# Kernel tuning notes

Hardware: AMD Instinct MI355X
Metric: run time of the kernel (lower is better)

Reference implementation:

```python
import jax, jax.numpy as jnp
import numpy as np
from jax import lax

B, E, T = 16, 512, 512
H, R = 1024, 32
P = 8192
W = 3            # window_size
MAX_SPAN = 8


def setup_inputs() -> dict:
    key = jax.random.key(0)
    ks = jax.random.split(key, 16)
    s = lambda fan: 1.0 / np.sqrt(fan)
    return {
        'rel_word_x': jax.random.normal(ks[0], (B, E, T), jnp.float32),
        'trig_attn': jax.random.normal(ks[1], (B, T), jnp.float32),
        'batch_idx': jax.random.randint(ks[2], (P,), 0, B),
        'head_index': jax.random.randint(ks[3], (P,), 0, T - MAX_SPAN),
        'head_span': jax.random.randint(ks[4], (P,), 1, MAX_SPAN + 1),
        'tail_index': jax.random.randint(ks[5], (P,), 0, T - MAX_SPAN),
        'tail_span': jax.random.randint(ks[6], (P,), 1, MAX_SPAN + 1),
        'rel_labels': jax.random.randint(ks[7], (P,), 0, R),
        'conv1_w': jax.random.uniform(ks[8], (E, E, W), jnp.float32, -s(E * W), s(E * W)),
        'conv1_b': jnp.zeros((E,), jnp.float32),
        'conv2_w': jax.random.uniform(ks[9], (E, E, W), jnp.float32, -s(E * W), s(E * W)),
        'conv2_b': jnp.zeros((E,), jnp.float32),
        'w1': jax.random.uniform(ks[10], (H, E), jnp.float32, -s(E), s(E)),
        'b1': jnp.zeros((H,), jnp.float32),
        'w2': jax.random.uniform(ks[11], (H, H), jnp.float32, -s(H), s(H)),
        'b2': jnp.zeros((H,), jnp.float32),
        'wr': jax.random.uniform(ks[12], (R, H), jnp.float32, -s(H), s(H)),
        'br': jnp.zeros((R,), jnp.float32),
    }


def _conv1d(x, w, b):
    # x: [B,E,T], w: [O,I,W] -> same-length conv (odd W)
    y = lax.conv_general_dilated(x, w, window_strides=(1,), padding=[(W // 2, W // 2)],
                                 dimension_numbers=('NCH', 'OIH', 'NCH'))
    return y + b[None, :, None]


def _span_max(x_bte, bidx, start, span):
    # x_bte: [B,T,E]; ragged span max via fixed-width gather + mask
    offs = jnp.arange(MAX_SPAN)
    pos = start[:, None] + offs[None, :]                  # [P,S]
    vals = x_bte[bidx[:, None], pos]                      # [P,S,E]
    mask = (offs[None, :] < span[:, None])[..., None]     # [P,S,1]
    return jnp.max(jnp.where(mask, vals, -jnp.inf), axis=1)  # [P,E]


def reference(rel_word_x, trig_attn, batch_idx, head_index, head_span,
              tail_index, tail_span, rel_labels,
              conv1_w, conv1_b, conv2_w, conv2_b, w1, b1, w2, b2, wr, br):
    # dropout treated as identity (eval-mode reference)
    x = rel_word_x
    x = jax.nn.relu(_conv1d(x, conv1_w, conv1_b)) + x
    x = jax.nn.relu(_conv1d(x, conv2_w, conv2_b)) + x
    x_bte = jnp.transpose(x, (0, 2, 1))                   # [B,T,E]
    headrep = _span_max(x_bte, batch_idx, head_index, head_span)
    tailrep = _span_max(x_bte, batch_idx, tail_index, tail_span)
    maxed = headrep + tailrep                             # [P,E]
    h = jax.nn.relu(maxed @ w1.T + b1)                    # [P,H]
    h = jax.nn.relu(h @ w2.T + b2)                        # [P,H]
    rel_logits = h @ wr.T + br                            # [P,R]
    return rel_logits, trig_attn, rel_labels
```

## Files before the change

### kernel.cpp

```cpp
#include <hip/hip_runtime.h>

typedef unsigned short u16;
typedef unsigned int u32;
typedef __attribute__((ext_vector_type(4))) float f32x4;
typedef __attribute__((ext_vector_type(8))) __bf16 bf16x8;
typedef __attribute__((ext_vector_type(4))) u16 u16x4;
typedef const __attribute__((address_space(1))) void* as1cv;
typedef __attribute__((address_space(3))) void* as3v;

static __device__ __forceinline__ float bf2f(u16 v) {
  union { u32 u; float f; } x; x.u = ((u32)v) << 16; return x.f;
}
static __device__ __forceinline__ u16 f2bf(float f) {
  union { float f; u32 u; } x; x.f = f;
  u32 r = x.u + 0x7FFFu + ((x.u >> 16) & 1u);
  return (u16)(r >> 16);
}


__global__ void __launch_bounds__(256) k_transpose(const float* __restrict__ x,
                                                   u16* __restrict__ xtp) {
  __shared__ float tile[32][33];
  const int b = blockIdx.z;
  const int t0 = blockIdx.x * 32, e0 = blockIdx.y * 32;
  const int tx = threadIdx.x & 31, ty = threadIdx.x >> 5;
  const float* src = x + (size_t)b * 512 * 512;
#pragma unroll
  for (int i = 0; i < 32; i += 8)
    tile[ty + i][tx] = src[(size_t)(e0 + ty + i) * 512 + t0 + tx];
  __syncthreads();
  u16* dst = xtp + (size_t)b * 514 * 512;
#pragma unroll
  for (int i = 0; i < 32; i += 8)
    dst[(size_t)(t0 + ty + i + 1) * 512 + e0 + tx] = f2bf(tile[tx][ty + i]);
}

__global__ void __launch_bounds__(256) k_prep(
    const float* __restrict__ wa, const float* __restrict__ wb,
    u16* __restrict__ ga, u16* __restrict__ gb,
    const float* __restrict__ w1, const float* __restrict__ w2,
    const float* __restrict__ wr, u16* __restrict__ wdst,
    u16* __restrict__ xtp0, u16* __restrict__ xtp1,
    const float* __restrict__ trig, const int* __restrict__ labels,
    float* __restrict__ out) {
  const int idx = blockIdx.x * 256 + threadIdx.x;
  {
    const float* w = (idx < 262144) ? wa : wb;
    u16* g = (idx < 262144) ? ga : gb;
    const int id = idx & 262143;
    const int o = id >> 9, i = id & 511;
    const float* p = w + (size_t)id * 3;
    g[(size_t)o * 1536 + i]        = f2bf(p[0]);
    g[(size_t)o * 1536 + 512 + i]  = f2bf(p[1]);
    g[(size_t)o * 1536 + 1024 + i] = f2bf(p[2]);
  }
  if (idx < 401408) {
    const int e0 = idx * 4;
    const float* src; int off;
    if (e0 < 524288)       { src = w1; off = e0; }
    else if (e0 < 1572864) { src = w2; off = e0 - 524288; }
    else                   { src = wr; off = e0 - 1572864; }
    const float4 v = *(const float4*)(src + off);
    u16x4 r; r.x = f2bf(v.x); r.y = f2bf(v.y); r.z = f2bf(v.z); r.w = f2bf(v.w);
    *(u16x4*)(wdst + e0) = r;
  }
  if (idx < 262144) out[idx] = 0.f;
  if (idx < 16384) {
    const int b = idx >> 10, rem = idx & 1023;
    const int row = (rem >> 9) ? 513 : 0, e = rem & 511;
    const size_t off = (size_t)b * 514 * 512 + (size_t)row * 512 + e;
    xtp0[off] = 0;
    xtp1[off] = 0;
  }
  if (idx < 8192) {
    out[262144 + idx] = trig[idx];
    out[270336 + idx] = (float)labels[idx];
  }
}

__global__ void __launch_bounds__(256) k_spanmax(const u16* __restrict__ xt2,
    const int* __restrict__ bidx, const int* __restrict__ hidx, const int* __restrict__ hspan,
    const int* __restrict__ tidx, const int* __restrict__ tspan, u16* __restrict__ maxed) {
  const int p = blockIdx.x;
  const int b = bidx[p], h0 = hidx[p], hn = hspan[p], t0 = tidx[p], tn = tspan[p];
  const u32* base = (const u32*)(xt2 + (size_t)b * 512 * 512);
  const int e = threadIdx.x;
  float m0 = -1e30f, m1 = -1e30f, q0 = -1e30f, q1 = -1e30f;
  for (int s = 0; s < hn; ++s) {
    const u32 v = base[(size_t)(h0 + s) * 256 + e];
    m0 = fmaxf(m0, bf2f((u16)v));
    m1 = fmaxf(m1, bf2f((u16)(v >> 16)));
  }
  for (int s = 0; s < tn; ++s) {
    const u32 v = base[(size_t)(t0 + s) * 256 + e];
    q0 = fmaxf(q0, bf2f((u16)v));
    q1 = fmaxf(q1, bf2f((u16)(v >> 16)));
  }
  const u32 r = (u32)f2bf(m0 + q0) | ((u32)f2bf(m1 + q1) << 16);
  ((u32*)(maxed + (size_t)p * 512))[e] = r;
}

template<int BM, int BN, int WM, int WN, int CONV, int RELU, int RESID, int OUTF32,
         int ATOMIC, int SWZ>
__global__ void __launch_bounds__(256, 2) k_gemm(
    const u16* __restrict__ A, int strideA, long long batchA,
    const u16* __restrict__ Bw, int strideB, long long batchB, int K,
    const float* __restrict__ bias,
    const u16* __restrict__ resid, long long batchR,
    void* __restrict__ outp, long long batchO, int strideO,
    int swz_nx, int swz_nyb, int swz_pp) {
  constexpr int FM = BM / (16 * WM);
  constexpr int FN = BN / (16 * WN);
  constexpr int CA = BM / 16, CB = BN / 16;
  __shared__ __align__(16) u16 lds[2][(BM + BN) * 32];
  const int tid = threadIdx.x;
  const int wave = tid >> 6, lane = tid & 63;
  int m0, n0, z;
  if constexpr (SWZ) {
    const int lin = blockIdx.x;
    const int xcd = lin & 7, slot = lin >> 3;
    const int xb = slot % swz_nx;
    const int p  = xcd * swz_pp + slot / swz_nx;
    m0 = (p % swz_nyb) * BM;
    n0 = xb * BN;
    z  = p / swz_nyb;
  } else {
    m0 = blockIdx.y * BM; n0 = blockIdx.x * BN; z = blockIdx.z;
  }
  const u16* Ab = A + (size_t)z * batchA;
  const u16* Bb = Bw + (size_t)z * batchB;
  const int NT = K >> 5;

  auto stage = [&](int t, int buf) {
    const int k0 = t << 5;
    const int arow = CONV ? (k0 >> 9) : 0;
    const int acol = CONV ? (k0 & 511) : k0;
    for (int c = wave; c < CA + CB; c += 4) {
      const u16* gsrc;
      u16* ldst;
      if (c < CA) {
        const int r0 = c << 4;
        ldst = &lds[buf][r0 * 32];
        const int row = m0 + r0 + (lane >> 2) + arow;
        gsrc = Ab + (size_t)row * strideA + acol + ((lane & 3) << 3);
      } else {
        const int r0 = (c - CA) << 4;
        ldst = &lds[buf][BM * 32 + r0 * 32];
        const int row = n0 + r0 + (lane >> 2);
        gsrc = Bb + (size_t)row * strideB + k0 + ((lane & 3) << 3);
      }
      __builtin_amdgcn_global_load_lds((as1cv)gsrc, (as3v)ldst, 16, 0, 0);
    }
  };

  f32x4 acc[FM][FN];
  const f32x4 zero4 = {0.f, 0.f, 0.f, 0.f};
#pragma unroll
  for (int m = 0; m < FM; ++m)
#pragma unroll
    for (int n = 0; n < FN; ++n) acc[m][n] = zero4;

  const int wrow = wave / WN, wcol = wave % WN;
  const int rsel = lane & 15;
  const int kc = (lane >> 4) << 3;

  stage(0, 0);
  __syncthreads();
  int cur = 0;
  for (int t = 0; t < NT; ++t) {
    if (t + 1 < NT) stage(t + 1, cur ^ 1);
    const u16* As = lds[cur];
    const u16* Bs = lds[cur] + BM * 32;
    bf16x8 af[FM], bq[FN];
#pragma unroll
    for (int m = 0; m < FM; ++m)
      af[m] = *(const bf16x8*)&As[(wrow * FM * 16 + m * 16 + rsel) * 32 + kc];
#pragma unroll
    for (int n = 0; n < FN; ++n)
      bq[n] = *(const bf16x8*)&Bs[(wcol * FN * 16 + n * 16 + rsel) * 32 + kc];
#pragma unroll
    for (int m = 0; m < FM; ++m)
#pragma unroll
      for (int n = 0; n < FN; ++n)
        acc[m][n] = __builtin_amdgcn_mfma_f32_16x16x32_bf16(af[m], bq[n], acc[m][n], 0, 0, 0);
    __syncthreads();
    cur ^= 1;
  }

  const int rowbase = m0 + wrow * FM * 16 + ((lane >> 4) << 2);
  const int colbase = n0 + wcol * FN * 16 + rsel;
  float bv[FN];
#pragma unroll
  for (int n = 0; n < FN; ++n)
    bv[n] = (!ATOMIC || z == 0) ? bias[colbase + n * 16] : 0.f;
  const u16* Rb = RESID ? (resid + (size_t)z * batchR) : (const u16*)nullptr;
  float* of = (float*)outp;
  u16* ob = (u16*)outp;
  const size_t obase = (size_t)z * batchO;
#pragma unroll
  for (int m = 0; m < FM; ++m) {
#pragma unroll
    for (int r = 0; r < 4; ++r) {
      const int row = rowbase + m * 16 + r;
#pragma unroll
      for (int n = 0; n < FN; ++n) {
        const int col = colbase + n * 16;
        float v = acc[m][n][r] + bv[n];
        if (RELU) v = fmaxf(v, 0.f);
        if (RESID) v += bf2f(Rb[(size_t)row * strideO + col]);
        const size_t o = obase + (size_t)row * strideO + col;
        if (ATOMIC) atomicAdd(&of[o], v);
        else if (OUTF32) of[o] = v;
        else ob[o] = f2bf(v);
      }
    }
  }
}

extern "C" void kernel_launch(void* const* d_in, const int* in_sizes, int n_in,
                              void* d_out, int out_size, void* d_ws, size_t ws_size,
                              hipStream_t stream) {
  const float* x    = (const float*)d_in[0];
  const float* trig = (const float*)d_in[1];
  const int* bidx   = (const int*)d_in[2];
  const int* hidx   = (const int*)d_in[3];
  const int* hspan  = (const int*)d_in[4];
  const int* tidx   = (const int*)d_in[5];
  const int* tspan  = (const int*)d_in[6];
  const int* labels = (const int*)d_in[7];
  const float* c1w  = (const float*)d_in[8];
  const float* c1b  = (const float*)d_in[9];
  const float* c2w  = (const float*)d_in[10];
  const float* c2b  = (const float*)d_in[11];
  const float* w1   = (const float*)d_in[12];
  const float* b1   = (const float*)d_in[13];
  const float* w2   = (const float*)d_in[14];
  const float* b2   = (const float*)d_in[15];
  const float* wrp  = (const float*)d_in[16];
  const float* br   = (const float*)d_in[17];
  float* out = (float*)d_out;
  char* ws = (char*)d_ws;
  (void)in_sizes; (void)n_in; (void)out_size; (void)ws_size;

  const size_t S_xtp = (size_t)16 * 514 * 512 * 2;
  u16* xtp0  = (u16*)(ws);
  u16* xtp1  = (u16*)(ws + S_xtp);
  u16* xt2   = (u16*)(ws);
  u16* maxed = (u16*)(ws + S_xtp);
  u16* h2    = (u16*)(ws);
  u16* h1    = (u16*)(ws + 2 * S_xtp);
  u16* wg1   = (u16*)(ws + 2 * S_xtp + (size_t)16 * 1024 * 1024);
  u16* wg2   = wg1 + (size_t)512 * 1536;
  u16* w1b   = wg2 + (size_t)512 * 1536;
  u16* w2b   = w1b + (size_t)1024 * 512;
  u16* wrb   = w2b + (size_t)1024 * 1024;

  k_transpose<<<dim3(16, 16, 16), 256, 0, stream>>>(x, xtp0);
  k_prep<<<2048, 256, 0, stream>>>(c1w, c2w, wg1, wg2, w1, w2, wrp, w1b,
                                   xtp0, xtp1, trig, labels, out);

  k_gemm<128, 64, 2, 2, 1, 1, 1, 0, 0, 1><<<512, 256, 0, stream>>>(
      xtp0, 512, (long long)514 * 512, wg1, 1536, 0, 1536, c1b,
      xtp0 + 512, (long long)514 * 512,
      xtp1 + 512, (long long)514 * 512, 512, 8, 4, 8);
  k_gemm<128, 64, 2, 2, 1, 1, 1, 0, 0, 1><<<512, 256, 0, stream>>>(
      xtp1, 512, (long long)514 * 512, wg2, 1536, 0, 1536, c2b,
      xtp1 + 512, (long long)514 * 512,
      xt2, (long long)512 * 512, 512, 8, 4, 8);

  k_spanmax<<<8192, 256, 0, stream>>>(xt2, bidx, hidx, hspan, tidx, tspan, maxed);

  k_gemm<128, 64, 2, 2, 0, 1, 0, 0, 0, 1><<<1024, 256, 0, stream>>>(
      maxed, 512, 0, w1b, 512, 0, 512, b1, nullptr, 0, h1, 0, 1024, 16, 64, 8);
  k_gemm<128, 128, 2, 2, 0, 1, 0, 0, 0, 1><<<512, 256, 0, stream>>>(
      h1, 1024, 0, w2b, 1024, 0, 1024, b2, nullptr, 0, h2, 0, 1024, 8, 64, 8);
  k_gemm<64, 32, 2, 2, 0, 0, 0, 1, 1, 0><<<dim3(1, 128, 4), 256, 0, stream>>>(
      h2, 1024, 256, wrb, 1024, 256, 256, br, nullptr, 0, out, 0, 32, 0, 0, 0);
}
```

Baseline: 247.2 us.

## Add dedicated conv kernel reusing shifted A tile across taps; widen GEMM K-step

A new conv kernel loads one A tile of 144 rows (128 plus halo) per K step, and all three weight taps read from it at row offsets. Each input row is therefore fetched from global memory once per K step instead of once per tap, as the generic GEMM did with K=1536. The generic GEMM gains a KS template parameter so the w2 GEMM can stage 64-wide K tiles, halving its barrier count. The cost is more LDS per block and a more complex staging layout.

```diff
diff --git a/kernel.cpp b/kernel.cpp
--- a/kernel.cpp
+++ b/kernel.cpp
@@ -100,19 +100,111 @@
   ((u32*)(maxed + (size_t)p * 512))[e] = r;
 }
 
-template<int BM, int BN, int WM, int WN, int CONV, int RELU, int RESID, int OUTF32,
-         int ATOMIC, int SWZ>
+__global__ void __launch_bounds__(256, 2) k_conv(
+    const u16* __restrict__ Abase,
+    const u16* __restrict__ Bw,
+    const float* __restrict__ bias,
+    u16* __restrict__ outbase,
+    long long batchA, long long batchO) {
+  constexpr int ASZ = 144 * 32;
+  __shared__ __align__(16) u16 lds[2][ASZ + 192 * 32];
+  const int tid = threadIdx.x, wave = tid >> 6, lane = tid & 63;
+  const int lin = blockIdx.x;
+  const int xcd = lin & 7, slot = lin >> 3;
+  const int n0 = (slot & 7) * 64;
+  const int p = xcd * 8 + (slot >> 3);
+  const int m0 = (p & 3) * 128;
+  const int z = p >> 2;
+  const u16* Ab = Abase + (size_t)z * batchA;
+  u16* outp = outbase + (size_t)z * batchO;
+
+  auto stage = [&](int t, int buf) {
+    const int k0 = t << 5;
+    for (int c = wave; c < 21; c += 4) {
+      const u16* gsrc; u16* ldst;
+      if (c < 9) {
+        ldst = &lds[buf][c * 512];
+        const int row = m0 + c * 16 + (lane >> 2);
+        gsrc = Ab + (size_t)row * 512 + k0 + ((lane & 3) << 3);
+      } else {
+        const int cb = c - 9, w = cb >> 2, r0 = (cb & 3) << 4;
+        ldst = &lds[buf][ASZ + (w * 64 + r0) * 32];
+        const int row = n0 + r0 + (lane >> 2);
+        gsrc = Bw + (size_t)row * 1536 + (w << 9) + k0 + ((lane & 3) << 3);
+      }
+      __builtin_amdgcn_global_load_lds((as1cv)gsrc, (as3v)ldst, 16, 0, 0);
+    }
+  };
+
+  f32x4 acc[4][2];
+  const f32x4 zero4 = {0.f, 0.f, 0.f, 0.f};
+#pragma unroll
+  for (int m = 0; m < 4; ++m)
+#pragma unroll
+    for (int n = 0; n < 2; ++n) acc[m][n] = zero4;
+
+  const int wrow = wave >> 1, wcol = wave & 1;
+  const int rsel = lane & 15, kc = (lane >> 4) << 3;
+
+  stage(0, 0);
+  __syncthreads();
+  int cur = 0;
+  for (int t = 0; t < 16; ++t) {
+    if (t + 1 < 16) stage(t + 1, cur ^ 1);
+    const u16* As = lds[cur];
+    const u16* Bs = lds[cur] + ASZ;
+#pragma unroll
+    for (int w = 0; w < 3; ++w) {
+      bf16x8 af[4], bq[2];
+#pragma unroll
+      for (int m = 0; m < 4; ++m)
+        af[m] = *(const bf16x8*)&As[(wrow * 64 + m * 16 + rsel + w) * 32 + kc];
+#pragma unroll
+      for (int n = 0; n < 2; ++n)
+        bq[n] = *(const bf16x8*)&Bs[(w * 64 + wcol * 32 + n * 16 + rsel) * 32 + kc];
+#pragma unroll
+      for (int m = 0; m < 4; ++m)
+#pragma unroll
+        for (int n = 0; n < 2; ++n)
+          acc[m][n] = __builtin_amdgcn_mfma_f32_16x16x32_bf16(af[m], bq[n], acc[m][n], 0, 0, 0);
+    }
+    __syncthreads();
+    cur ^= 1;
+  }
+
+  const int rowbase = m0 + wrow * 64 + ((lane >> 4) << 2);
+  const int colbase = n0 + wcol * 32 + rsel;
+  const float bv0 = bias[colbase], bv1 = bias[colbase + 16];
+  const u16* Rb = Ab + 512;
+#pragma unroll
+  for (int m = 0; m < 4; ++m) {
+#pragma unroll
+    for (int r = 0; r < 4; ++r) {
+      const int row = rowbase + m * 16 + r;
+#pragma unroll
+      for (int n = 0; n < 2; ++n) {
+        const int col = colbase + n * 16;
+        float v = fmaxf(acc[m][n][r] + (n ? bv1 : bv0), 0.f);
+        v += bf2f(Rb[(size_t)row * 512 + col]);
+        outp[(size_t)row * 512 + col] = f2bf(v);
+      }
+    }
+  }
+}
+
+template<int BM, int BN, int WM, int WN, int KS, int RELU, int OUTF32, int ATOMIC, int SWZ>
 __global__ void __launch_bounds__(256, 2) k_gemm(
     const u16* __restrict__ A, int strideA, long long batchA,
     const u16* __restrict__ Bw, int strideB, long long batchB, int K,
     const float* __restrict__ bias,
-    const u16* __restrict__ resid, long long batchR,
     void* __restrict__ outp, long long batchO, int strideO,
     int swz_nx, int swz_nyb, int swz_pp) {
   constexpr int FM = BM / (16 * WM);
   constexpr int FN = BN / (16 * WN);
-  constexpr int CA = BM / 16, CB = BN / 16;
-  __shared__ __align__(16) u16 lds[2][(BM + BN) * 32];
+  constexpr int LPR = KS / 8;
+  constexpr int RPC = 64 / LPR;
+  constexpr int NCH = (BM + BN) / RPC;
+  __shared__ __align__(16) u16 lds[2][(BM + BN) * KS];
   const int tid = threadIdx.x;
   const int wave = tid >> 6, lane = tid & 63;
   int m0, n0, z;
@@ -129,27 +221,18 @@
   }
   const u16* Ab = A + (size_t)z * batchA;
   const u16* Bb = Bw + (size_t)z * batchB;
-  const int NT = K >> 5;
+  const int NT = K / KS;
 
   auto stage = [&](int t, int buf) {
-    const int k0 = t << 5;
-    const int arow = CONV ? (k0 >> 9) : 0;
-    const int acol = CONV ? (k0 & 511) : k0;
-    for (int c = wave; c < CA + CB; c += 4) {
-      const u16* gsrc;
-      u16* ldst;
-      if (c < CA) {
-        const int r0 = c << 4;
-        ldst = &lds[buf][r0 * 32];
-        const int row = m0 + r0 + (lane >> 2) + arow;
-        gsrc = Ab + (size_t)row * strideA + acol + ((lane & 3) << 3);
-      } else {
-        const int r0 = (c - CA) << 4;
-        ldst = &lds[buf][BM * 32 + r0 * 32];
-        const int row = n0 + r0 + (lane >> 2);
-        gsrc = Bb + (size_t)row * strideB + k0 + ((lane & 3) << 3);
-      }
-      __builtin_amdgcn_global_load_lds((as1cv)gsrc, (as3v)ldst, 16, 0, 0);
+    const int k0 = t * KS;
+    const int lrow = lane / LPR, lcol = (lane % LPR) << 3;
+    for (int c = wave; c < NCH; c += 4) {
+      const int gr = c * RPC + lrow;
+      const bool isA = gr < BM;
+      const int row = isA ? (m0 + gr) : (n0 + gr - BM);
+      const u16* gsrc = (isA ? Ab + (size_t)row * strideA : Bb + (size_t)row * strideB)
+                        + k0 + lcol;
+      __builtin_amdgcn_global_load_lds((as1cv)gsrc, (as3v)&lds[buf][c * 512], 16, 0, 0);
     }
   };
 
@@ -170,19 +253,22 @@
   for (int t = 0; t < NT; ++t) {
     if (t + 1 < NT) stage(t + 1, cur ^ 1);
     const u16* As = lds[cur];
-    const u16* Bs = lds[cur] + BM * 32;
-    bf16x8 af[FM], bq[FN];
-#pragma unroll
-    for (int m = 0; m < FM; ++m)
-      af[m] = *(const bf16x8*)&As[(wrow * FM * 16 + m * 16 + rsel) * 32 + kc];
-#pragma unroll
-    for (int n = 0; n < FN; ++n)
-      bq[n] = *(const bf16x8*)&Bs[(wcol * FN * 16 + n * 16 + rsel) * 32 + kc];
-#pragma unroll
-    for (int m = 0; m < FM; ++m)
+    const u16* Bs = lds[cur] + BM * KS;
+#pragma unroll
+    for (int ks = 0; ks < KS / 32; ++ks) {
+      bf16x8 af[FM], bq[FN];
+#pragma unroll
+      for (int m = 0; m < FM; ++m)
+        af[m] = *(const bf16x8*)&As[(wrow * FM * 16 + m * 16 + rsel) * KS + ks * 32 + kc];
 #pragma unroll
       for (int n = 0; n < FN; ++n)
-        acc[m][n] = __builtin_amdgcn_mfma_f32_16x16x32_bf16(af[m], bq[n], acc[m][n], 0, 0, 0);
+        bq[n] = *(const bf16x8*)&Bs[(wcol * FN * 16 + n * 16 + rsel) * KS + ks * 32 + kc];
+#pragma unroll
+      for (int m = 0; m < FM; ++m)
+#pragma unroll
+        for (int n = 0; n < FN; ++n)
+          acc[m][n] = __builtin_amdgcn_mfma_f32_16x16x32_bf16(af[m], bq[n], acc[m][n], 0, 0, 0);
+    }
     __syncthreads();
     cur ^= 1;
   }
@@ -193,7 +279,6 @@
 #pragma unroll
   for (int n = 0; n < FN; ++n)
     bv[n] = (!ATOMIC || z == 0) ? bias[colbase + n * 16] : 0.f;
-  const u16* Rb = RESID ? (resid + (size_t)z * batchR) : (const u16*)nullptr;
   float* of = (float*)outp;
   u16* ob = (u16*)outp;
   const size_t obase = (size_t)z * batchO;
@@ -207,7 +292,6 @@
         const int col = colbase + n * 16;
         float v = acc[m][n][r] + bv[n];
         if (RELU) v = fmaxf(v, 0.f);
-        if (RESID) v += bf2f(Rb[(size_t)row * strideO + col]);
         const size_t o = obase + (size_t)row * strideO + col;
         if (ATOMIC) atomicAdd(&of[o], v);
         else if (OUTF32) of[o] = v;
@@ -259,21 +343,17 @@
   k_prep<<<2048, 256, 0, stream>>>(c1w, c2w, wg1, wg2, w1, w2, wrp, w1b,
                                    xtp0, xtp1, trig, labels, out);
 
-  k_gemm<128, 64, 2, 2, 1, 1, 1, 0, 0, 1><<<512, 256, 0, stream>>>(
-      xtp0, 512, (long long)514 * 512, wg1, 1536, 0, 1536, c1b,
-      xtp0 + 512, (long long)514 * 512,
-      xtp1 + 512, (long long)514 * 512, 512, 8, 4, 8);
-  k_gemm<128, 64, 2, 2, 1, 1, 1, 0, 0, 1><<<512, 256, 0, stream>>>(
-      xtp1, 512, (long long)514 * 512, wg2, 1536, 0, 1536, c2b,
-      xtp1 + 512, (long long)514 * 512,
-      xt2, (long long)512 * 512, 512, 8, 4, 8);
+  k_conv<<<512, 256, 0, stream>>>(xtp0, wg1, c1b, xtp1 + 512,
+                                  (long long)514 * 512, (long long)514 * 512);
+  k_conv<<<512, 256, 0, stream>>>(xtp1, wg2, c2b, xt2,
+                                  (long long)514 * 512, (long long)512 * 512);
 
   k_spanmax<<<8192, 256, 0, stream>>>(xt2, bidx, hidx, hspan, tidx, tspan, maxed);
 
-  k_gemm<128, 64, 2, 2, 0, 1, 0, 0, 0, 1><<<1024, 256, 0, stream>>>(
-      maxed, 512, 0, w1b, 512, 0, 512, b1, nullptr, 0, h1, 0, 1024, 16, 64, 8);
-  k_gemm<128, 128, 2, 2, 0, 1, 0, 0, 0, 1><<<512, 256, 0, stream>>>(
-      h1, 1024, 0, w2b, 1024, 0, 1024, b2, nullptr, 0, h2, 0, 1024, 8, 64, 8);
-  k_gemm<64, 32, 2, 2, 0, 0, 0, 1, 1, 0><<<dim3(1, 128, 4), 256, 0, stream>>>(
-      h2, 1024, 256, wrb, 1024, 256, 256, br, nullptr, 0, out, 0, 32, 0, 0, 0);
-}
+  k_gemm<128, 64, 2, 2, 32, 1, 0, 0, 1><<<1024, 256, 0, stream>>>(
+      maxed, 512, 0, w1b, 512, 0, 512, b1, h1, 0, 1024, 16, 64, 8);
+  k_gemm<128, 128, 2, 2, 64, 1, 0, 0, 1><<<512, 256, 0, stream>>>(
+      h1, 1024, 0, w2b, 1024, 0, 1024, b2, h2, 0, 1024, 8, 64, 8);
+  k_gemm<64, 32, 2, 2, 32, 0, 1, 1, 0><<<dim3(1, 128, 4), 256, 0, stream>>>(
+      h2, 1024, 256, wrb, 1024, 256, 256, br, out, 0, 32, 0, 0, 0);
+}
```

Result: faster. 225.0 us (-9.0%).
